# Kernel tuning notes

Measured on AMD Instinct MI355X. Metric: run time of the kernel, lower is better.

## Reference

```python
import jax, jax.numpy as jnp
import numpy as np

INPUT_DIM = 512
EMBED_DIM = 512
N_HEAD = 8
HEAD_DIM = EMBED_DIM // N_HEAD


def setup_inputs() -> dict:
    key = jax.random.key(0)
    k0, k1, k2 = jax.random.split(key, 3)
    B, S = 2, 4096
    X = jax.random.normal(k0, (B, S, INPUT_DIM), dtype=jnp.float32)
    # xavier_uniform for Linear weights (torch weight shape [out, in])
    def xavier(k, out_f, in_f):
        bound = float(np.sqrt(6.0 / (in_f + out_f)))
        return jax.random.uniform(k, (out_f, in_f), jnp.float32, -bound, bound)
    W_qkv = xavier(k1, 3 * EMBED_DIM, INPUT_DIM)
    b_qkv = jnp.zeros((3 * EMBED_DIM,), jnp.float32)
    W_o = xavier(k2, EMBED_DIM, EMBED_DIM)
    b_o = jnp.zeros((EMBED_DIM,), jnp.float32)
    return {"X": X, "W_qkv": W_qkv, "b_qkv": b_qkv, "W_o": W_o, "b_o": b_o}


def reference(X, W_qkv, b_qkv, W_o, b_o):
    B, S, _ = X.shape
    # fused QKV projection: [B,S,3E]
    qkv = jnp.einsum("bsd,ed->bse", X, W_qkv) + b_qkv
    # [B,S,H,3*hd] -> [B,H,S,3*hd]
    qkv = qkv.reshape(B, S, N_HEAD, 3 * HEAD_DIM).transpose(0, 2, 1, 3)
    q, k, v = jnp.split(qkv, 3, axis=-1)
    scale = 1.0 / jnp.sqrt(jnp.asarray(HEAD_DIM, q.dtype))
    logits = jnp.einsum("bhqd,bhkd->bhqk", q, k) * scale  # [B,H,S,S]
    attn = jax.nn.softmax(logits, axis=-1)
    vals = jnp.einsum("bhqk,bhkd->bhqd", attn, v)
    vals = vals.transpose(0, 2, 1, 3).reshape(B, S, EMBED_DIM)
    out = jnp.einsum("bse,fe->bsf", vals, W_o) + b_o
    return out
```

## Files before the change

kernel.cpp:

```cpp
#include <hip/hip_runtime.h>

#define S_   4096
#define D_IN 512
#define E_   512
#define HD   64

typedef __attribute__((ext_vector_type(8))) short short8;
typedef __attribute__((ext_vector_type(16))) float f32x16;

#define MFMA32(a, b, c) __builtin_amdgcn_mfma_f32_32x32x16_bf16((a), (b), (c), 0, 0, 0)

__device__ __forceinline__ unsigned short f2bf(float f) {
  unsigned u = __builtin_bit_cast(unsigned, f);
  u = (u + 0x7FFFu + ((u >> 16) & 1u)) >> 16;
  return (unsigned short)u;
}

__device__ __forceinline__ unsigned cvt_pk_bf16(float lo, float hi) {
  unsigned r;
  asm("v_cvt_pk_bf16_f32 %0, %1, %2" : "=v"(r) : "v"(lo), "v"(hi));
  return r;
}

__device__ __forceinline__ f32x16 splat16(float x) {
  f32x16 v;
#pragma unroll
  for (int i = 0; i < 16; ++i) v[i] = x;
  return v;
}

__global__ __launch_bounds__(256) void cvt_f32_bf16(const float* __restrict__ src,
                                                    unsigned short* __restrict__ dst,
                                                    int n4) {
  int i = blockIdx.x * 256 + threadIdx.x;
  if (i < n4) {
    float4 v = reinterpret_cast<const float4*>(src)[i];
    ushort4 o;
    o.x = f2bf(v.x); o.y = f2bf(v.y); o.z = f2bf(v.z); o.w = f2bf(v.w);
    reinterpret_cast<ushort4*>(dst)[i] = o;
  }
}

__global__ __launch_bounds__(256, 3) void qkv_proj(const unsigned short* __restrict__ Xb,
                                                   const unsigned short* __restrict__ Wb,
                                                   const float* __restrict__ bias,
                                                   unsigned short* __restrict__ Qb,
                                                   unsigned short* __restrict__ Kb,
                                                   unsigned short* __restrict__ Vt) {
  __shared__ unsigned short Al[128][72];
  __shared__ unsigned short Bl[128][72];
  const int tid = threadIdx.x;
  const int w = tid >> 6, l = tid & 63, h = l >> 5, r31 = l & 31;
  const int wm = w >> 1, wn = w & 1;
  const int m0 = blockIdx.x * 128, n0 = blockIdx.y * 128;
  const int sr = tid >> 1, sc = tid & 1;

  f32x16 a00 = {}, a01 = {}, a10 = {}, a11 = {};
  const unsigned short* ap = Xb + (size_t)(m0 + sr) * D_IN + sc * 32;
  const unsigned short* bp = Wb + (size_t)(n0 + sr) * D_IN + sc * 32;
  for (int k0 = 0; k0 < D_IN; k0 += 64) {
    int4 av0 = *reinterpret_cast<const int4*>(ap + k0);
    int4 av1 = *reinterpret_cast<const int4*>(ap + k0 + 8);
    int4 av2 = *reinterpret_cast<const int4*>(ap + k0 + 16);
    int4 av3 = *reinterpret_cast<const int4*>(ap + k0 + 24);
    int4 bv0 = *reinterpret_cast<const int4*>(bp + k0);
    int4 bv1 = *reinterpret_cast<const int4*>(bp + k0 + 8);
    int4 bv2 = *reinterpret_cast<const int4*>(bp + k0 + 16);
    int4 bv3 = *reinterpret_cast<const int4*>(bp + k0 + 24);
    __syncthreads();
    *reinterpret_cast<int4*>(&Al[sr][sc * 32])      = av0;
    *reinterpret_cast<int4*>(&Al[sr][sc * 32 + 8])  = av1;
    *reinterpret_cast<int4*>(&Al[sr][sc * 32 + 16]) = av2;
    *reinterpret_cast<int4*>(&Al[sr][sc * 32 + 24]) = av3;
    *reinterpret_cast<int4*>(&Bl[sr][sc * 32])      = bv0;
    *reinterpret_cast<int4*>(&Bl[sr][sc * 32 + 8])  = bv1;
    *reinterpret_cast<int4*>(&Bl[sr][sc * 32 + 16]) = bv2;
    *reinterpret_cast<int4*>(&Bl[sr][sc * 32 + 24]) = bv3;
    __syncthreads();
#pragma unroll
    for (int c = 0; c < 4; ++c) {
      short8 aA = *reinterpret_cast<const short8*>(&Al[wm * 64 + r31][c * 16 + h * 8]);
      short8 aB = *reinterpret_cast<const short8*>(&Al[wm * 64 + 32 + r31][c * 16 + h * 8]);
      short8 bA = *reinterpret_cast<const short8*>(&Bl[wn * 64 + r31][c * 16 + h * 8]);
      short8 bB = *reinterpret_cast<const short8*>(&Bl[wn * 64 + 32 + r31][c * 16 + h * 8]);
      a00 = MFMA32(aA, bA, a00);
      a01 = MFMA32(aA, bB, a01);
      a10 = MFMA32(aB, bA, a10);
      a11 = MFMA32(aB, bB, a11);
    }
  }
#pragma unroll
  for (int rb = 0; rb < 2; ++rb)
#pragma unroll
    for (int cb = 0; cb < 2; ++cb) {
      const f32x16 A = rb ? (cb ? a11 : a10) : (cb ? a01 : a00);
      int n = n0 + wn * 64 + cb * 32 + r31;
      int hh = n / 192;
      int j = n - hh * 192;
      int t3 = j >> 6;
      int d = j & 63;
      float bn = bias[n];
      int mbase0 = m0 + wm * 64 + rb * 32 + h * 4;
#pragma unroll
      for (int rq = 0; rq < 4; ++rq) {
        int mb = mbase0 + rq * 8;
        int bb = mb >> 12;
        int ssb = mb & 4095;
        int bhh = bb * 8 + hh;
        if (t3 == 0) {
#pragma unroll
          for (int i = 0; i < 4; ++i)
            Qb[((size_t)bhh * S_ + ssb + i) * HD + d] =
                f2bf((A[rq * 4 + i] + bn) * (0.125f * 1.44269504088896f));
        } else if (t3 == 1) {
#pragma unroll
          for (int i = 0; i < 4; ++i)
            Kb[((size_t)bhh * S_ + ssb + i) * HD + d] = f2bf(A[rq * 4 + i] + bn);
        } else {
          int sp = (ssb & ~12) | ((ssb & 8) >> 1) | ((ssb & 4) << 1);
          ushort4 o;
          o.x = f2bf(A[rq * 4 + 0] + bn);
          o.y = f2bf(A[rq * 4 + 1] + bn);
          o.z = f2bf(A[rq * 4 + 2] + bn);
          o.w = f2bf(A[rq * 4 + 3] + bn);
          *reinterpret_cast<ushort4*>(&Vt[((size_t)bhh * HD + d) * S_ + sp]) = o;
        }
      }
    }
}

__global__ __launch_bounds__(256, 2) void attn_fwd(const unsigned short* __restrict__ Qb,
                                                   const unsigned short* __restrict__ Kb,
                                                   const unsigned short* __restrict__ Vt,
                                                   unsigned short* __restrict__ vals) {
  __shared__ unsigned short Kl[64][72];
  __shared__ unsigned short Vl[64][72];
  const int tid = threadIdx.x;
  const int w = tid >> 6, l = tid & 63, h = l >> 5, r31 = l & 31;
  const int bh = blockIdx.x >> 5;
  const int q0 = (blockIdx.x & 31) * 128;
  const int sr = tid >> 2, sc = tid & 3;

  const int qrow = q0 + w * 32 + r31;
  const unsigned short* qp = Qb + ((size_t)bh * S_ + qrow) * HD + h * 8;
  short8 bq[4];
#pragma unroll
  for (int c = 0; c < 4; ++c)
    bq[c] = *reinterpret_cast<const short8*>(qp + c * 16);

  f32x16 po0 = {}, po1 = {};
  float lacc = 0.f;

  const unsigned short* kptr = Kb + ((size_t)bh * S_ + sr) * HD + sc * 16;
  const unsigned short* vptr = Vt + ((size_t)bh * HD + sr) * S_ + sc * 16;

  int4 kA = *reinterpret_cast<const int4*>(kptr);
  int4 kB = *reinterpret_cast<const int4*>(kptr + 8);
  int4 vA = *reinterpret_cast<const int4*>(vptr);
  int4 vB = *reinterpret_cast<const int4*>(vptr + 8);

  for (int kt = 0; kt < 64; ++kt) {
    __syncthreads();
    *reinterpret_cast<int4*>(&Kl[sr][sc * 16])     = kA;
    *reinterpret_cast<int4*>(&Kl[sr][sc * 16 + 8]) = kB;
    *reinterpret_cast<int4*>(&Vl[sr][sc * 16])     = vA;
    *reinterpret_cast<int4*>(&Vl[sr][sc * 16 + 8]) = vB;
    __syncthreads();

    if (kt < 63) {
      const unsigned short* kp = kptr + (size_t)(kt + 1) * 64 * HD;
      const unsigned short* vp = vptr + (kt + 1) * 64;
      kA = *reinterpret_cast<const int4*>(kp);
      kB = *reinterpret_cast<const int4*>(kp + 8);
      vA = *reinterpret_cast<const int4*>(vp);
      vB = *reinterpret_cast<const int4*>(vp + 8);
    }

    f32x16 s0 = splat16(-16.f), s1 = splat16(-16.f);
#pragma unroll
    for (int c = 0; c < 4; ++c) {
      short8 k0 = *reinterpret_cast<const short8*>(&Kl[r31][c * 16 + h * 8]);
      s0 = MFMA32(k0, bq[c], s0);
      short8 k1 = *reinterpret_cast<const short8*>(&Kl[32 + r31][c * 16 + h * 8]);
      s1 = MFMA32(k1, bq[c], s1);
    }

#pragma unroll
    for (int i = 0; i < 16; ++i) {
      s0[i] = __builtin_amdgcn_exp2f(s0[i]);
      s1[i] = __builtin_amdgcn_exp2f(s1[i]);
    }
    float r0 = ((s0[0] + s0[1]) + (s0[2] + s0[3])) + ((s0[4] + s0[5]) + (s0[6] + s0[7]));
    float r1 = ((s0[8] + s0[9]) + (s0[10] + s0[11])) + ((s0[12] + s0[13]) + (s0[14] + s0[15]));
    float r2 = ((s1[0] + s1[1]) + (s1[2] + s1[3])) + ((s1[4] + s1[5]) + (s1[6] + s1[7]));
    float r3 = ((s1[8] + s1[9]) + (s1[10] + s1[11])) + ((s1[12] + s1[13]) + (s1[14] + s1[15]));
    lacc += (r0 + r1) + (r2 + r3);

#pragma unroll
    for (int c = 0; c < 4; ++c) {
      const f32x16 pp = (c < 2) ? s0 : s1;
      const int o8 = (c & 1) * 8;
      uint4 pk;
      pk.x = cvt_pk_bf16(pp[o8 + 0], pp[o8 + 1]);
      pk.y = cvt_pk_bf16(pp[o8 + 2], pp[o8 + 3]);
      pk.z = cvt_pk_bf16(pp[o8 + 4], pp[o8 + 5]);
      pk.w = cvt_pk_bf16(pp[o8 + 6], pp[o8 + 7]);
      short8 pf = __builtin_bit_cast(short8, pk);
      short8 v0 = *reinterpret_cast<const short8*>(&Vl[r31][c * 16 + h * 8]);
      po0 = MFMA32(v0, pf, po0);
      short8 v1 = *reinterpret_cast<const short8*>(&Vl[32 + r31][c * 16 + h * 8]);
      po1 = MFMA32(v1, pf, po1);
    }
  }

  float lt = lacc + __shfl_xor(lacc, 32);
  float inv = 1.0f / lt;
  const int b = bh >> 3, hd = bh & 7;
  unsigned short* op = vals + ((size_t)b * S_ + qrow) * E_ + hd * HD + h * 4;
#pragma unroll
  for (int db = 0; db < 2; ++db) {
    const f32x16 P = db ? po1 : po0;
#pragma unroll
    for (int rq = 0; rq < 4; ++rq) {
      ushort4 o;
      o.x = f2bf(P[rq * 4 + 0] * inv);
      o.y = f2bf(P[rq * 4 + 1] * inv);
      o.z = f2bf(P[rq * 4 + 2] * inv);
      o.w = f2bf(P[rq * 4 + 3] * inv);
      *reinterpret_cast<ushort4*>(op + db * 32 + rq * 8) = o;
    }
  }
}

__global__ __launch_bounds__(256, 3) void o_proj(const unsigned short* __restrict__ Ab,
                                                 const unsigned short* __restrict__ Wb,
                                                 const float* __restrict__ bias,
                                                 float* __restrict__ out) {
  __shared__ unsigned short Al[128][72];
  __shared__ unsigned short Bl[128][72];
  const int tid = threadIdx.x;
  const int w = tid >> 6, l = tid & 63, h = l >> 5, r31 = l & 31;
  const int wm = w >> 1, wn = w & 1;
  const int m0 = blockIdx.x * 128, n0 = blockIdx.y * 128;
  const int sr = tid >> 1, sc = tid & 1;

  f32x16 a00 = {}, a01 = {}, a10 = {}, a11 = {};
  const unsigned short* ap = Ab + (size_t)(m0 + sr) * E_ + sc * 32;
  const unsigned short* bp = Wb + (size_t)(n0 + sr) * E_ + sc * 32;
  for (int k0 = 0; k0 < E_; k0 += 64) {
    int4 av0 = *reinterpret_cast<const int4*>(ap + k0);
    int4 av1 = *reinterpret_cast<const int4*>(ap + k0 + 8);
    int4 av2 = *reinterpret_cast<const int4*>(ap + k0 + 16);
    int4 av3 = *reinterpret_cast<const int4*>(ap + k0 + 24);
    int4 bv0 = *reinterpret_cast<const int4*>(bp + k0);
    int4 bv1 = *reinterpret_cast<const int4*>(bp + k0 + 8);
    int4 bv2 = *reinterpret_cast<const int4*>(bp + k0 + 16);
    int4 bv3 = *reinterpret_cast<const int4*>(bp + k0 + 24);
    __syncthreads();
    *reinterpret_cast<int4*>(&Al[sr][sc * 32])      = av0;
    *reinterpret_cast<int4*>(&Al[sr][sc * 32 + 8])  = av1;
    *reinterpret_cast<int4*>(&Al[sr][sc * 32 + 16]) = av2;
    *reinterpret_cast<int4*>(&Al[sr][sc * 32 + 24]) = av3;
    *reinterpret_cast<int4*>(&Bl[sr][sc * 32])      = bv0;
    *reinterpret_cast<int4*>(&Bl[sr][sc * 32 + 8])  = bv1;
    *reinterpret_cast<int4*>(&Bl[sr][sc * 32 + 16]) = bv2;
    *reinterpret_cast<int4*>(&Bl[sr][sc * 32 + 24]) = bv3;
    __syncthreads();
#pragma unroll
    for (int c = 0; c < 4; ++c) {
      short8 aA = *reinterpret_cast<const short8*>(&Al[wm * 64 + r31][c * 16 + h * 8]);
      short8 aB = *reinterpret_cast<const short8*>(&Al[wm * 64 + 32 + r31][c * 16 + h * 8]);
      short8 bA = *reinterpret_cast<const short8*>(&Bl[wn * 64 + r31][c * 16 + h * 8]);
      short8 bB = *reinterpret_cast<const short8*>(&Bl[wn * 64 + 32 + r31][c * 16 + h * 8]);
      a00 = MFMA32(aA, bA, a00);
      a01 = MFMA32(aA, bB, a01);
      a10 = MFMA32(aB, bA, a10);
      a11 = MFMA32(aB, bB, a11);
    }
  }
#pragma unroll
  for (int rb = 0; rb < 2; ++rb)
#pragma unroll
    for (int cb = 0; cb < 2; ++cb) {
      const f32x16 A = rb ? (cb ? a11 : a10) : (cb ? a01 : a00);
      int n = n0 + wn * 64 + cb * 32 + r31;
      float bn = bias[n];
      int mbase0 = m0 + wm * 64 + rb * 32 + h * 4;
#pragma unroll
      for (int rq = 0; rq < 4; ++rq)
#pragma unroll
        for (int i = 0; i < 4; ++i)
          out[(size_t)(mbase0 + rq * 8 + i) * E_ + n] = A[rq * 4 + i] + bn;
    }
}

extern "C" void kernel_launch(void* const* d_in, const int* in_sizes, int n_in,
                              void* d_out, int out_size, void* d_ws, size_t ws_size,
                              hipStream_t stream) {
  const float* X    = (const float*)d_in[0];
  const float* Wqkv = (const float*)d_in[1];
  const float* bqkv = (const float*)d_in[2];
  const float* Wo   = (const float*)d_in[3];
  const float* bo   = (const float*)d_in[4];
  float* out = (float*)d_out;

  char* ws = (char*)d_ws;
  unsigned short* Xb   = (unsigned short*)(ws);
  unsigned short* Wqb  = (unsigned short*)(ws + 8388608);
  unsigned short* Wob  = (unsigned short*)(ws + 9961472);
  unsigned short* Qb   = (unsigned short*)(ws + 10485760);
  unsigned short* Kb   = (unsigned short*)(ws + 18874368);
  unsigned short* Vt   = (unsigned short*)(ws + 27262976);
  unsigned short* vals = (unsigned short*)(ws + 35651584);

  cvt_f32_bf16<<<4096, 256, 0, stream>>>(X, Xb, 4194304 / 4);
  cvt_f32_bf16<<<768, 256, 0, stream>>>(Wqkv, Wqb, 786432 / 4);
  cvt_f32_bf16<<<256, 256, 0, stream>>>(Wo, Wob, 262144 / 4);

  qkv_proj<<<dim3(64, 12), 256, 0, stream>>>(Xb, Wqb, bqkv, Qb, Kb, Vt);
  attn_fwd<<<512, 256, 0, stream>>>(Qb, Kb, Vt, vals);
  o_proj<<<dim3(64, 4), 256, 0, stream>>>(vals, Wob, bo, out);
}
```

Before: 132.1 us.

## Split attention KV range across two wave groups, double-buffer LDS, fuse conversions

```diff
diff --git a/kernel.cpp b/kernel.cpp
--- a/kernel.cpp
+++ b/kernel.cpp
@@ -29,16 +29,23 @@
   return v;
 }
 
-__global__ __launch_bounds__(256) void cvt_f32_bf16(const float* __restrict__ src,
-                                                    unsigned short* __restrict__ dst,
-                                                    int n4) {
-  int i = blockIdx.x * 256 + threadIdx.x;
-  if (i < n4) {
-    float4 v = reinterpret_cast<const float4*>(src)[i];
-    ushort4 o;
-    o.x = f2bf(v.x); o.y = f2bf(v.y); o.z = f2bf(v.z); o.w = f2bf(v.w);
-    reinterpret_cast<ushort4*>(dst)[i] = o;
-  }
+__global__ __launch_bounds__(256) void cvt3(const float* __restrict__ X,
+                                            const float* __restrict__ Wq,
+                                            const float* __restrict__ Wo,
+                                            unsigned short* __restrict__ Xb,
+                                            unsigned short* __restrict__ Wqb,
+                                            unsigned short* __restrict__ Wob) {
+  int bid = blockIdx.x;
+  const float* src;
+  unsigned short* dst;
+  int i;
+  if (bid < 4096)      { src = X;  dst = Xb;  i = bid * 256 + threadIdx.x; }
+  else if (bid < 4864) { src = Wq; dst = Wqb; i = (bid - 4096) * 256 + threadIdx.x; }
+  else                 { src = Wo; dst = Wob; i = (bid - 4864) * 256 + threadIdx.x; }
+  float4 v = reinterpret_cast<const float4*>(src)[i];
+  ushort4 o;
+  o.x = f2bf(v.x); o.y = f2bf(v.y); o.z = f2bf(v.z); o.w = f2bf(v.w);
+  reinterpret_cast<ushort4*>(dst)[i] = o;
 }
 
 __global__ __launch_bounds__(256, 3) void qkv_proj(const unsigned short* __restrict__ Xb,
@@ -129,19 +136,26 @@
     }
 }
 
-__global__ __launch_bounds__(256, 2) void attn_fwd(const unsigned short* __restrict__ Qb,
+__global__ __launch_bounds__(512, 4) void attn_fwd(const unsigned short* __restrict__ Qb,
                                                    const unsigned short* __restrict__ Kb,
                                                    const unsigned short* __restrict__ Vt,
                                                    unsigned short* __restrict__ vals) {
-  __shared__ unsigned short Kl[64][72];
-  __shared__ unsigned short Vl[64][72];
+  __shared__ char smem[73728];
   const int tid = threadIdx.x;
   const int w = tid >> 6, l = tid & 63, h = l >> 5, r31 = l & 31;
+  const int grp = w >> 2;
+  const int wq = w & 3;
   const int bh = blockIdx.x >> 5;
   const int q0 = (blockIdx.x & 31) * 128;
-  const int sr = tid >> 2, sc = tid & 3;
-
-  const int qrow = q0 + w * 32 + r31;
+  const int lt256 = tid & 255;
+  const int sr = lt256 >> 2, sc = lt256 & 3;
+
+  unsigned short (*Kl)[64][72] =
+      reinterpret_cast<unsigned short(*)[64][72]>(smem + grp * 36864);
+  unsigned short (*Vl)[64][72] =
+      reinterpret_cast<unsigned short(*)[64][72]>(smem + grp * 36864 + 18432);
+
+  const int qrow = q0 + wq * 32 + r31;
   const unsigned short* qp = Qb + ((size_t)bh * S_ + qrow) * HD + h * 8;
   short8 bq[4];
 #pragma unroll
@@ -151,23 +165,26 @@
   f32x16 po0 = {}, po1 = {};
   float lacc = 0.f;
 
-  const unsigned short* kptr = Kb + ((size_t)bh * S_ + sr) * HD + sc * 16;
-  const unsigned short* vptr = Vt + ((size_t)bh * HD + sr) * S_ + sc * 16;
-
-  int4 kA = *reinterpret_cast<const int4*>(kptr);
-  int4 kB = *reinterpret_cast<const int4*>(kptr + 8);
-  int4 vA = *reinterpret_cast<const int4*>(vptr);
-  int4 vB = *reinterpret_cast<const int4*>(vptr + 8);
-
-  for (int kt = 0; kt < 64; ++kt) {
-    __syncthreads();
-    *reinterpret_cast<int4*>(&Kl[sr][sc * 16])     = kA;
-    *reinterpret_cast<int4*>(&Kl[sr][sc * 16 + 8]) = kB;
-    *reinterpret_cast<int4*>(&Vl[sr][sc * 16])     = vA;
-    *reinterpret_cast<int4*>(&Vl[sr][sc * 16 + 8]) = vB;
-    __syncthreads();
-
-    if (kt < 63) {
+  const int kvbase = grp * 2048;
+  const unsigned short* kptr = Kb + ((size_t)bh * S_ + kvbase + sr) * HD + sc * 16;
+  const unsigned short* vptr = Vt + ((size_t)bh * HD + sr) * S_ + kvbase + sc * 16;
+
+  {
+    int4 kA = *reinterpret_cast<const int4*>(kptr);
+    int4 kB = *reinterpret_cast<const int4*>(kptr + 8);
+    int4 vA = *reinterpret_cast<const int4*>(vptr);
+    int4 vB = *reinterpret_cast<const int4*>(vptr + 8);
+    *reinterpret_cast<int4*>(&Kl[0][sr][sc * 16])     = kA;
+    *reinterpret_cast<int4*>(&Kl[0][sr][sc * 16 + 8]) = kB;
+    *reinterpret_cast<int4*>(&Vl[0][sr][sc * 16])     = vA;
+    *reinterpret_cast<int4*>(&Vl[0][sr][sc * 16 + 8]) = vB;
+  }
+  __syncthreads();
+
+  for (int kt = 0; kt < 32; ++kt) {
+    const int cur = kt & 1;
+    int4 kA, kB, vA, vB;
+    if (kt < 31) {
       const unsigned short* kp = kptr + (size_t)(kt + 1) * 64 * HD;
       const unsigned short* vp = vptr + (kt + 1) * 64;
       kA = *reinterpret_cast<const int4*>(kp);
@@ -179,9 +196,9 @@
     f32x16 s0 = splat16(-16.f), s1 = splat16(-16.f);
 #pragma unroll
     for (int c = 0; c < 4; ++c) {
-      short8 k0 = *reinterpret_cast<const short8*>(&Kl[r31][c * 16 + h * 8]);
+      short8 k0 = *reinterpret_cast<const short8*>(&Kl[cur][r31][c * 16 + h * 8]);
       s0 = MFMA32(k0, bq[c], s0);
-      short8 k1 = *reinterpret_cast<const short8*>(&Kl[32 + r31][c * 16 + h * 8]);
+      short8 k1 = *reinterpret_cast<const short8*>(&Kl[cur][32 + r31][c * 16 + h * 8]);
       s1 = MFMA32(k1, bq[c], s1);
     }
 
@@ -206,28 +223,55 @@
       pk.z = cvt_pk_bf16(pp[o8 + 4], pp[o8 + 5]);
       pk.w = cvt_pk_bf16(pp[o8 + 6], pp[o8 + 7]);
       short8 pf = __builtin_bit_cast(short8, pk);
-      short8 v0 = *reinterpret_cast<const short8*>(&Vl[r31][c * 16 + h * 8]);
+      short8 v0 = *reinterpret_cast<const short8*>(&Vl[cur][r31][c * 16 + h * 8]);
       po0 = MFMA32(v0, pf, po0);
-      short8 v1 = *reinterpret_cast<const short8*>(&Vl[32 + r31][c * 16 + h * 8]);
+      short8 v1 = *reinterpret_cast<const short8*>(&Vl[cur][32 + r31][c * 16 + h * 8]);
       po1 = MFMA32(v1, pf, po1);
     }
-  }
-
-  float lt = lacc + __shfl_xor(lacc, 32);
-  float inv = 1.0f / lt;
-  const int b = bh >> 3, hd = bh & 7;
-  unsigned short* op = vals + ((size_t)b * S_ + qrow) * E_ + hd * HD + h * 4;
-#pragma unroll
-  for (int db = 0; db < 2; ++db) {
-    const f32x16 P = db ? po1 : po0;
-#pragma unroll
-    for (int rq = 0; rq < 4; ++rq) {
-      ushort4 o;
-      o.x = f2bf(P[rq * 4 + 0] * inv);
-      o.y = f2bf(P[rq * 4 + 1] * inv);
-      o.z = f2bf(P[rq * 4 + 2] * inv);
-      o.w = f2bf(P[rq * 4 + 3] * inv);
-      *reinterpret_cast<ushort4*>(op + db * 32 + rq * 8) = o;
+
+    if (kt < 31) {
+      *reinterpret_cast<int4*>(&Kl[cur ^ 1][sr][sc * 16])     = kA;
+      *reinterpret_cast<int4*>(&Kl[cur ^ 1][sr][sc * 16 + 8]) = kB;
+      *reinterpret_cast<int4*>(&Vl[cur ^ 1][sr][sc * 16])     = vA;
+      *reinterpret_cast<int4*>(&Vl[cur ^ 1][sr][sc * 16 + 8]) = vB;
+    }
+    __syncthreads();
+  }
+
+  float ltp = lacc + __shfl_xor(lacc, 32);
+  float* Ox = reinterpret_cast<float*>(smem);
+  float* lx = reinterpret_cast<float*>(smem + 34816);
+  const int qlocal = wq * 32 + r31;
+  if (grp == 0) {
+#pragma unroll
+    for (int db = 0; db < 2; ++db) {
+      const f32x16 P = db ? po1 : po0;
+#pragma unroll
+      for (int rq = 0; rq < 4; ++rq) {
+        float4 st = {P[rq * 4 + 0], P[rq * 4 + 1], P[rq * 4 + 2], P[rq * 4 + 3]};
+        *reinterpret_cast<float4*>(&Ox[qlocal * 68 + db * 32 + rq * 8 + h * 4]) = st;
+      }
+    }
+    if (h == 0) lx[qlocal] = ltp;
+  }
+  __syncthreads();
+  if (grp == 1) {
+    float inv = 1.0f / (ltp + lx[qlocal]);
+    const int b = bh >> 3, hd = bh & 7;
+    unsigned short* op = vals + ((size_t)b * S_ + qrow) * E_ + hd * HD + h * 4;
+#pragma unroll
+    for (int db = 0; db < 2; ++db) {
+      const f32x16 P = db ? po1 : po0;
+#pragma unroll
+      for (int rq = 0; rq < 4; ++rq) {
+        float4 pv = *reinterpret_cast<const float4*>(&Ox[qlocal * 68 + db * 32 + rq * 8 + h * 4]);
+        ushort4 o;
+        o.x = f2bf((P[rq * 4 + 0] + pv.x) * inv);
+        o.y = f2bf((P[rq * 4 + 1] + pv.y) * inv);
+        o.z = f2bf((P[rq * 4 + 2] + pv.z) * inv);
+        o.w = f2bf((P[rq * 4 + 3] + pv.w) * inv);
+        *reinterpret_cast<ushort4*>(op + db * 32 + rq * 8) = o;
+      }
     }
   }
 }
@@ -313,11 +357,8 @@
   unsigned short* Vt   = (unsigned short*)(ws + 27262976);
   unsigned short* vals = (unsigned short*)(ws + 35651584);
 
-  cvt_f32_bf16<<<4096, 256, 0, stream>>>(X, Xb, 4194304 / 4);
-  cvt_f32_bf16<<<768, 256, 0, stream>>>(Wqkv, Wqb, 786432 / 4);
-  cvt_f32_bf16<<<256, 256, 0, stream>>>(Wo, Wob, 262144 / 4);
-
+  cvt3<<<5120, 256, 0, stream>>>(X, Wqkv, Wo, Xb, Wqb, Wob);
   qkv_proj<<<dim3(64, 12), 256, 0, stream>>>(Xb, Wqb, bqkv, Qb, Kb, Vt);
-  attn_fwd<<<512, 256, 0, stream>>>(Qb, Kb, Vt, vals);
+  attn_fwd<<<512, 512, 0, stream>>>(Qb, Kb, Vt, vals);
   o_proj<<<dim3(64, 4), 256, 0, stream>>>(vals, Wob, bo, out);
 }
```

After: 126.0 us. 4.6% less time.
